# Optimization experiments

Measured on AMD Instinct MI355X. Metric: run time of the kernel, lower is better.

Reference implementation:

```python
import jax, jax.numpy as jnp
import numpy as np

N, CS, CZ = 512, 384, 128
H, C, PQ, PV = 12, 16, 4, 8
NB = 8
EPS = 1e-8


def _ln(x, g, b):
    m = jnp.mean(x, axis=-1, keepdims=True)
    v = jnp.mean((x - m) ** 2, axis=-1, keepdims=True)
    return (x - m) / jnp.sqrt(v + 1e-5) * g + b


def _quat_rot(bcd):
    # (1, b, c, d) quaternion -> rotation matrix, as in AF2 BackboneUpdate
    ones = jnp.ones(bcd.shape[:-1] + (1,), bcd.dtype)
    q = jnp.concatenate([ones, bcd], axis=-1)
    q = q / jnp.linalg.norm(q, axis=-1, keepdims=True)
    w, x, y, z = q[..., 0], q[..., 1], q[..., 2], q[..., 3]
    R = jnp.stack([
        1 - 2 * (y * y + z * z), 2 * (x * y - w * z), 2 * (x * z + w * y),
        2 * (x * y + w * z), 1 - 2 * (x * x + z * z), 2 * (y * z - w * x),
        2 * (x * z - w * y), 2 * (y * z + w * x), 1 - 2 * (x * x + y * y),
    ], axis=-1)
    return R.reshape(bcd.shape[:-1] + (3, 3))


def _ipa(s, z, R, t, p):
    n = s.shape[0]
    q = (s @ p['w_q']).reshape(n, H, C)
    kv = (s @ p['w_kv']).reshape(n, H, 2, C)
    k, v = kv[..., 0, :], kv[..., 1, :]

    # local points -> global frames
    q_pts = (s @ p['w_qpts']).reshape(n, H * PQ, 3)
    q_pts = jnp.einsum('nxy,npy->npx', R, q_pts) + t[:, None, :]
    q_pts = q_pts.reshape(n, H, PQ, 3)
    kv_pts = (s @ p['w_kvpts']).reshape(n, H * (PQ + PV), 3)
    kv_pts = jnp.einsum('nxy,npy->npx', R, kv_pts) + t[:, None, :]
    kv_pts = kv_pts.reshape(n, H, PQ + PV, 3)
    k_pts, v_pts = kv_pts[:, :, :PQ], kv_pts[:, :, PQ:]

    b = z @ p['w_b']  # [i, j, H]

    scalar = jnp.einsum('ihc,jhc->hij', q, k) / np.sqrt(C)
    # sum_p ||q_ip - k_jp||^2 expanded to avoid [N,N,H,P,3] intermediate
    sq_q = jnp.sum(q_pts ** 2, axis=(-1, -2)).T  # [H, i]
    sq_k = jnp.sum(k_pts ** 2, axis=(-1, -2)).T  # [H, j]
    cross = jnp.einsum('ihpc,jhpc->hij', q_pts, k_pts)
    d2 = sq_q[:, :, None] + sq_k[:, None, :] - 2.0 * cross  # [H, i, j]

    gamma = jax.nn.softplus(p['head_weights'])  # [H]
    w_C = np.sqrt(2.0 / (9.0 * PQ))
    w_L = np.sqrt(1.0 / 3.0)
    logits = w_L * (scalar + jnp.transpose(b, (2, 0, 1))
                    - gamma[:, None, None] * (w_C / 2.0) * d2)
    a = jax.nn.softmax(logits, axis=-1)  # [H, i, j]

    o = jnp.einsum('hij,jhc->ihc', a, v).reshape(n, H * C)
    o_pt = jnp.einsum('hij,jhpc->ihpc', a, v_pts)
    # back to local frame: R_i^{-1} (o_pt - t_i)
    o_pt = jnp.einsum('nyx,nhpy->nhpx', R, o_pt - t[:, None, None, :])
    o_pt_norm = jnp.sqrt(jnp.sum(o_pt ** 2, axis=-1) + EPS)  # [n, H, PV]
    o_pair = jnp.einsum('hij,ijz->ihz', a, z).reshape(n, H * CZ)

    cat = jnp.concatenate([o, o_pt.reshape(n, H * PV * 3),
                           o_pt_norm.reshape(n, H * PV), o_pair], axis=-1)
    return cat @ p['w_out'] + p['b_out']


def _forward(s, z, p):
    n = s.shape[0]
    R = jnp.broadcast_to(jnp.eye(3, dtype=s.dtype), (n, 3, 3))
    t = jnp.zeros((n, 3), s.dtype)
    for _ in range(NB):  # shared weights across blocks, as in AF2
        s = s + _ipa(s, z, R, t, p)
        s = _ln(s, p['ln1_g'], p['ln1_b'])
        h = jax.nn.relu(s @ p['w_t1'])
        h = jax.nn.relu(h @ p['w_t2'])
        s = s + h @ p['w_t3']
        s = _ln(s, p['ln2_g'], p['ln2_b'])
        upd = s @ p['w_bb'] + p['b_bb']  # [n, 6]
        Ru = _quat_rot(upd[:, :3])
        tu = upd[:, 3:]
        t = jnp.einsum('nxy,ny->nx', R, tu) + t
        R = jnp.einsum('nxy,nyz->nxz', R, Ru)
    return jnp.concatenate([s, t], axis=-1)  # [n, CS + 3]


def setup_inputs() -> dict:
    key = jax.random.key(0)
    ks = jax.random.split(key, 12)
    sc = 0.02
    cat_dim = H * C + H * PV * 3 + H * PV + H * CZ  # 2112
    return {
        's': jax.random.normal(ks[0], (N, CS), jnp.float32),
        'z': jax.random.normal(ks[1], (N, N, CZ), jnp.float32),
        'w_q': jax.random.normal(ks[2], (CS, H * C), jnp.float32) * sc,
        'w_kv': jax.random.normal(ks[3], (CS, H * 2 * C), jnp.float32) * sc,
        'w_qpts': jax.random.normal(ks[4], (CS, H * PQ * 3), jnp.float32) * sc,
        'w_kvpts': jax.random.normal(ks[5], (CS, H * (PQ + PV) * 3), jnp.float32) * sc,
        'w_b': jax.random.normal(ks[6], (CZ, H), jnp.float32) * sc,
        'head_weights': jnp.zeros((H,), jnp.float32),
        'w_out': jax.random.normal(ks[7], (cat_dim, CS), jnp.float32) * sc,
        'b_out': jnp.zeros((CS,), jnp.float32),
        'ln1_g': jnp.ones((CS,), jnp.float32),
        'ln1_b': jnp.zeros((CS,), jnp.float32),
        'w_t1': jax.random.normal(ks[8], (CS, CS), jnp.float32) * sc,
        'w_t2': jax.random.normal(ks[9], (CS, CS), jnp.float32) * sc,
        'w_t3': jax.random.normal(ks[10], (CS, CS), jnp.float32) * sc,
        'ln2_g': jnp.ones((CS,), jnp.float32),
        'ln2_b': jnp.zeros((CS,), jnp.float32),
        'w_bb': jax.random.normal(ks[11], (CS, 6), jnp.float32) * sc,
        'b_bb': jnp.zeros((6,), jnp.float32),
    }


def reference(s, z, w_q, w_kv, w_qpts, w_kvpts, w_b, head_weights, w_out,
              b_out, ln1_g, ln1_b, w_t1, w_t2, w_t3, ln2_g, ln2_b, w_bb, b_bb):
    p = dict(w_q=w_q, w_kv=w_kv, w_qpts=w_qpts, w_kvpts=w_kvpts, w_b=w_b,
             head_weights=head_weights, w_out=w_out, b_out=b_out,
             ln1_g=ln1_g, ln1_b=ln1_b, w_t1=w_t1, w_t2=w_t2, w_t3=w_t3,
             ln2_g=ln2_g, ln2_b=ln2_b, w_bb=w_bb, b_bb=b_bb)
    return _forward(s, z, p)
```

## Files before the change

### kernel.cpp

```cpp
#include <hip/hip_runtime.h>
#include <hip/hip_bf16.h>

constexpr int Nres = 512;
constexpr int Cs   = 384;
constexpr int Cz   = 128;
constexpr int NH   = 12;
constexpr int HC   = 16;
constexpr int NPQ  = 4;
constexpr int NPV  = 8;
constexpr int NBLK = 8;
constexpr int PROJD = NH*HC + NH*2*HC + NH*NPQ*3 + NH*(NPQ+NPV)*3;
constexpr int CATD = NH*HC + NH*NPV*3 + NH*NPV + NH*Cz;
constexpr float W_L  = 0.57735026918962576f;
constexpr float W_C2 = 0.11785113019775793f;

using u16 = unsigned short;
typedef __bf16 bf16x8 __attribute__((ext_vector_type(8)));
typedef float  f32x4  __attribute__((ext_vector_type(4)));

static inline int gdiv(int n, int b) { return (n + b - 1) / b; }

static __device__ __forceinline__ u16 f2bf(float x) {
    __hip_bfloat16 h = __float2bfloat16(x);
    return *reinterpret_cast<u16*>(&h);
}
static __device__ __forceinline__ float bf2f(u16 x) {
    return __bfloat162float(*reinterpret_cast<__hip_bfloat16*>(&x));
}

__global__ void k_init(const float* __restrict__ s_in, float* __restrict__ s_cur,
                       u16* __restrict__ s_bf,
                       float* __restrict__ R, float* __restrict__ t) {
    int idx = blockIdx.x * blockDim.x + threadIdx.x;
    if (idx < Nres * Cs) { float v = s_in[idx]; s_cur[idx] = v; s_bf[idx] = f2bf(v); }
    if (idx < Nres * 9) {
        int e = idx % 9;
        R[idx] = (e == 0 || e == 4 || e == 8) ? 1.f : 0.f;
    }
    if (idx < Nres * 3) t[idx] = 0.f;
}

__global__ void k_concatW(const float* __restrict__ w_q, const float* __restrict__ w_kv,
                          const float* __restrict__ w_qpts, const float* __restrict__ w_kvpts,
                          float* __restrict__ Wcat) {
    int idx = blockIdx.x * blockDim.x + threadIdx.x;
    if (idx >= Cs * PROJD) return;
    int k = idx / PROJD, n = idx - k * PROJD;
    float v;
    if      (n < 192) v = w_q[k * 192 + n];
    else if (n < 576) v = w_kv[k * 384 + (n - 192)];
    else if (n < 720) v = w_qpts[k * 144 + (n - 576)];
    else              v = w_kvpts[k * 432 + (n - 720)];
    Wcat[idx] = v;
}

__global__ void k_transposeW(const float* __restrict__ in, u16* __restrict__ out,
                             int K, int N) {
    __shared__ float tile[32][33];
    int n0 = blockIdx.x * 32, k0 = blockIdx.y * 32;
    int tx = threadIdx.x & 31, ty = threadIdx.x >> 5;
#pragma unroll
    for (int j = 0; j < 4; j++)
        tile[ty + j * 8][tx] = in[(size_t)(k0 + ty + j * 8) * N + n0 + tx];
    __syncthreads();
#pragma unroll
    for (int j = 0; j < 4; j++)
        out[(size_t)(n0 + ty + j * 8) * K + k0 + tx] = f2bf(tile[tx][ty + j * 8]);
}

__global__ void k_zT(const float* __restrict__ z, u16* __restrict__ zT) {
    __shared__ float tile[32][33];
    int i  = blockIdx.x;
    int j0 = blockIdx.y * 32;
    int c0 = blockIdx.z * 32;
    int tx = threadIdx.x & 31, ty = threadIdx.x >> 5;
    const float* src = z + (size_t)i * Nres * Cz;
#pragma unroll
    for (int l = 0; l < 4; l++)
        tile[ty + l * 8][tx] = src[(size_t)(j0 + ty + l * 8) * Cz + c0 + tx];
    __syncthreads();
    u16* dst = zT + (size_t)i * Cz * Nres;
#pragma unroll
    for (int l = 0; l < 4; l++)
        dst[(size_t)(c0 + ty + l * 8) * Nres + j0 + tx] = f2bf(tile[tx][ty + l * 8]);
}

__global__ void __launch_bounds__(256)
k_gemm_mfma(const u16* __restrict__ A, const u16* __restrict__ Bt,
            float* __restrict__ P, int M, int K, int N, int Kc) {
    __shared__ u16 As[64 * 40];
    __shared__ u16 Bs[64 * 40];
    const int tid = threadIdx.x;
    const int m0 = blockIdx.y * 64;
    const int n0 = blockIdx.x * 64;
    const int kbeg = blockIdx.z * Kc;
    const int wv = tid >> 6, lane = tid & 63;
    const int wm = (wv >> 1) * 32, wn = (wv & 1) * 32;
    const int lrow = lane & 15, lq = lane >> 4;

    f32x4 zero = {0.f, 0.f, 0.f, 0.f};
    f32x4 acc00 = zero, acc01 = zero, acc10 = zero, acc11 = zero;

    const int srow = tid >> 2;
    const int sko  = (tid & 3) * 8;

    for (int k0 = kbeg; k0 < kbeg + Kc; k0 += 32) {
        *(uint4*)&As[srow * 40 + sko] = *(const uint4*)&A[(size_t)(m0 + srow) * K + k0 + sko];
        *(uint4*)&Bs[srow * 40 + sko] = *(const uint4*)&Bt[(size_t)(n0 + srow) * K + k0 + sko];
        __syncthreads();
        bf16x8 a0 = *reinterpret_cast<const bf16x8*>(&As[(wm + lrow) * 40 + lq * 8]);
        bf16x8 a1 = *reinterpret_cast<const bf16x8*>(&As[(wm + 16 + lrow) * 40 + lq * 8]);
        bf16x8 b0 = *reinterpret_cast<const bf16x8*>(&Bs[(wn + lrow) * 40 + lq * 8]);
        bf16x8 b1 = *reinterpret_cast<const bf16x8*>(&Bs[(wn + 16 + lrow) * 40 + lq * 8]);
        acc00 = __builtin_amdgcn_mfma_f32_16x16x32_bf16(a0, b0, acc00, 0, 0, 0);
        acc01 = __builtin_amdgcn_mfma_f32_16x16x32_bf16(a0, b1, acc01, 0, 0, 0);
        acc10 = __builtin_amdgcn_mfma_f32_16x16x32_bf16(a1, b0, acc10, 0, 0, 0);
        acc11 = __builtin_amdgcn_mfma_f32_16x16x32_bf16(a1, b1, acc11, 0, 0, 0);
        __syncthreads();
    }
    float* Pp = P + (size_t)blockIdx.z * M * N;
    const int rbase = m0 + wm + lq * 4;
    const int cbase = n0 + wn + lrow;
#pragma unroll
    for (int r = 0; r < 4; r++) {
        Pp[(size_t)(rbase + r) * N + cbase]           = acc00[r];
        Pp[(size_t)(rbase + r) * N + cbase + 16]      = acc01[r];
        Pp[(size_t)(rbase + 16 + r) * N + cbase]      = acc10[r];
        Pp[(size_t)(rbase + 16 + r) * N + cbase + 16] = acc11[r];
    }
}

__global__ void __launch_bounds__(256)
k_gemm_rbf(const u16* __restrict__ A, const u16* __restrict__ Bt,
           float* __restrict__ outf, u16* __restrict__ outb,
           int M, int K, int N, int relu_bf) {
    __shared__ u16 As[32 * 40];
    __shared__ u16 Bs[64 * 40];
    const int tid = threadIdx.x;
    const int m0 = blockIdx.y * 32;
    const int n0 = blockIdx.x * 64;
    const int wv = tid >> 6, lane = tid & 63;
    const int wm = (wv >> 1) * 16, wn = (wv & 1) * 32;
    const int lrow = lane & 15, lq = lane >> 4;
    f32x4 zero = {0.f, 0.f, 0.f, 0.f};
    f32x4 acc0 = zero, acc1 = zero;
    const int srow = tid >> 2, sko = (tid & 3) * 8;
    for (int k0 = 0; k0 < K; k0 += 32) {
        if (tid < 128)
            *(uint4*)&As[srow * 40 + sko] = *(const uint4*)&A[(size_t)(m0 + srow) * K + k0 + sko];
        *(uint4*)&Bs[srow * 40 + sko] = *(const uint4*)&Bt[(size_t)(n0 + srow) * K + k0 + sko];
        __syncthreads();
        bf16x8 a  = *reinterpret_cast<const bf16x8*>(&As[(wm + lrow) * 40 + lq * 8]);
        bf16x8 b0 = *reinterpret_cast<const bf16x8*>(&Bs[(wn + lrow) * 40 + lq * 8]);
        bf16x8 b1 = *reinterpret_cast<const bf16x8*>(&Bs[(wn + 16 + lrow) * 40 + lq * 8]);
        acc0 = __builtin_amdgcn_mfma_f32_16x16x32_bf16(a, b0, acc0, 0, 0, 0);
        acc1 = __builtin_amdgcn_mfma_f32_16x16x32_bf16(a, b1, acc1, 0, 0, 0);
        __syncthreads();
    }
    const int rbase = m0 + wm + lq * 4;
    const int cbase = n0 + wn + lrow;
    if (relu_bf) {
#pragma unroll
        for (int r = 0; r < 4; r++) {
            outb[(size_t)(rbase + r) * N + cbase]      = f2bf(fmaxf(acc0[r], 0.f));
            outb[(size_t)(rbase + r) * N + cbase + 16] = f2bf(fmaxf(acc1[r], 0.f));
        }
    } else {
#pragma unroll
        for (int r = 0; r < 4; r++) {
            outf[(size_t)(rbase + r) * N + cbase]      = acc0[r];
            outf[(size_t)(rbase + r) * N + cbase + 16] = acc1[r];
        }
    }
}

__global__ void k_bproj(const float* __restrict__ z, const float* __restrict__ w_b,
                        float* __restrict__ b_hij) {
    __shared__ float zs[16][129];
    __shared__ float wbs[Cz * NH];
    const int tid = threadIdx.x;
    const int base = blockIdx.x * 16;
#pragma unroll
    for (int l = 0; l < 6; l++) {
        int idx = tid + l * 256;
        if (idx < Cz * NH) wbs[idx] = w_b[idx];
    }
#pragma unroll
    for (int l = 0; l < 8; l++) {
        int idx = tid + l * 256;
        int r = idx >> 7, c = idx & 127;
        zs[r][c] = z[(size_t)(base + r) * Cz + c];
    }
    __syncthreads();
    if (tid < 192) {
        int h = tid >> 4, r = tid & 15;
        float acc = 0.f;
        for (int c = 0; c < Cz; c++) acc += zs[r][c] * wbs[c * NH + h];
        int row = base + r;
        int i = row >> 9, j = row & 511;
        b_hij[((size_t)h * Nres + i) * Nres + j] = acc * W_L;
    }
}

__global__ void k_prep(const float* __restrict__ proj, const float* __restrict__ R,
                       const float* __restrict__ t, const float* __restrict__ hw,
                       u16* __restrict__ Aaug, u16* __restrict__ Baug,
                       u16* __restrict__ vhT) {
    int idx = blockIdx.x * blockDim.x + threadIdx.x;
    if (idx >= NH * Nres) return;
    int h = idx / Nres, i = idx % Nres;
    float R_[9], t_[3];
#pragma unroll
    for (int e = 0; e < 9; e++) R_[e] = R[i * 9 + e];
#pragma unroll
    for (int e = 0; e < 3; e++) t_[e] = t[i * 3 + e];
    const float* prow = proj + (size_t)i * PROJD;
    float gam = log1pf(__expf(hw[h]));
    float ch  = sqrtf(2.f * gam * W_C2);

    u16 arow[32], brow[32];
#pragma unroll
    for (int c = 0; c < HC; c++) {
        arow[c] = f2bf(prow[h * HC + c] * (W_L * 0.25f));
        brow[c] = f2bf(prow[192 + h * 2 * HC + c]);
        vhT[((size_t)h * 48 + c) * Nres + i] = f2bf(prow[192 + h * 2 * HC + HC + c]);
    }
#pragma unroll
    for (int p = 0; p < NPQ; p++) {
        const float* src = prow + 576 + (h * NPQ + p) * 3;
        float y0 = src[0], y1 = src[1], y2 = src[2];
        float v0 = R_[0]*y0 + R_[1]*y1 + R_[2]*y2 + t_[0];
        float v1 = R_[3]*y0 + R_[4]*y1 + R_[5]*y2 + t_[1];
        float v2 = R_[6]*y0 + R_[7]*y1 + R_[8]*y2 + t_[2];
        float s = W_L * ch;
        arow[16 + p*3 + 0] = f2bf(v0 * s);
        arow[16 + p*3 + 1] = f2bf(v1 * s);
        arow[16 + p*3 + 2] = f2bf(v2 * s);
    }
    float sk = 0.f;
#pragma unroll
    for (int p = 0; p < NPQ + NPV; p++) {
        const float* src = prow + 720 + (h * (NPQ+NPV) + p) * 3;
        float y0 = src[0], y1 = src[1], y2 = src[2];
        float v0 = R_[0]*y0 + R_[1]*y1 + R_[2]*y2 + t_[0];
        float v1 = R_[3]*y0 + R_[4]*y1 + R_[5]*y2 + t_[1];
        float v2 = R_[6]*y0 + R_[7]*y1 + R_[8]*y2 + t_[2];
        if (p < NPQ) {
            brow[16 + p*3 + 0] = f2bf(v0 * ch);
            brow[16 + p*3 + 1] = f2bf(v1 * ch);
            brow[16 + p*3 + 2] = f2bf(v2 * ch);
            sk += v0*v0 + v1*v1 + v2*v2;
        } else {
            int c0 = 16 + (p - NPQ) * 3;
            vhT[((size_t)h * 48 + c0 + 0) * Nres + i] = f2bf(v0);
            vhT[((size_t)h * 48 + c0 + 1) * Nres + i] = f2bf(v1);
            vhT[((size_t)h * 48 + c0 + 2) * Nres + i] = f2bf(v2);
        }
    }
    float x = -W_L * gam * W_C2 * sk;
    u16 hi = f2bf(x);
    float lo = x - bf2f(hi);
    arow[28] = f2bf(1.0f); arow[29] = f2bf(1.0f); arow[30] = 0; arow[31] = 0;
    brow[28] = hi;         brow[29] = f2bf(lo);   brow[30] = 0; brow[31] = 0;

    uint4* ad = (uint4*)&Aaug[((size_t)h * Nres + i) * 32];
    uint4* bd = (uint4*)&Baug[((size_t)h * Nres + i) * 32];
    const uint4* as = (const uint4*)arow;
    const uint4* bs = (const uint4*)brow;
#pragma unroll
    for (int e = 0; e < 4; e++) { ad[e] = as[e]; bd[e] = bs[e]; }
}

__global__ void __launch_bounds__(256)
k_qk(const u16* __restrict__ Aaug, const u16* __restrict__ Baug,
     const float* __restrict__ b_hij, float* __restrict__ S) {
    __shared__ u16 As[64 * 40];
    __shared__ u16 Bs[64 * 40];
    const int tid = threadIdx.x;
    const int h  = blockIdx.z;
    const int i0 = blockIdx.y * 64;
    const int j0 = blockIdx.x * 64;
    const int wv = tid >> 6, lane = tid & 63;
    const int wm = (wv >> 1) * 32, wn = (wv & 1) * 32;
    const int lrow = lane & 15, lq = lane >> 4;
    const int srow = tid >> 2, sko = (tid & 3) * 8;

    *(uint4*)&As[srow * 40 + sko] = *(const uint4*)&Aaug[((size_t)h * Nres + i0 + srow) * 32 + sko];
    *(uint4*)&Bs[srow * 40 + sko] = *(const uint4*)&Baug[((size_t)h * Nres + j0 + srow) * 32 + sko];
    __syncthreads();

    f32x4 zero = {0.f, 0.f, 0.f, 0.f};
    bf16x8 a0 = *reinterpret_cast<const bf16x8*>(&As[(wm + lrow) * 40 + lq * 8]);
    bf16x8 a1 = *reinterpret_cast<const bf16x8*>(&As[(wm + 16 + lrow) * 40 + lq * 8]);
    bf16x8 b0 = *reinterpret_cast<const bf16x8*>(&Bs[(wn + lrow) * 40 + lq * 8]);
    bf16x8 b1 = *reinterpret_cast<const bf16x8*>(&Bs[(wn + 16 + lrow) * 40 + lq * 8]);
    f32x4 acc00 = __builtin_amdgcn_mfma_f32_16x16x32_bf16(a0, b0, zero, 0, 0, 0);
    f32x4 acc01 = __builtin_amdgcn_mfma_f32_16x16x32_bf16(a0, b1, zero, 0, 0, 0);
    f32x4 acc10 = __builtin_amdgcn_mfma_f32_16x16x32_bf16(a1, b0, zero, 0, 0, 0);
    f32x4 acc11 = __builtin_amdgcn_mfma_f32_16x16x32_bf16(a1, b1, zero, 0, 0, 0);

    const float* bh = b_hij + ((size_t)h * Nres + i0) * Nres + j0;
    float* Sp = S + ((size_t)h * Nres + i0) * Nres + j0;
    const int rbase = wm + lq * 4;
    const int cbase = wn + lrow;
#pragma unroll
    for (int r = 0; r < 4; r++) {
        Sp[(size_t)(rbase + r) * Nres + cbase]           = acc00[r] + bh[(size_t)(rbase + r) * Nres + cbase];
        Sp[(size_t)(rbase + r) * Nres + cbase + 16]      = acc01[r] + bh[(size_t)(rbase + r) * Nres + cbase + 16];
        Sp[(size_t)(rbase + 16 + r) * Nres + cbase]      = acc10[r] + bh[(size_t)(rbase + 16 + r) * Nres + cbase];
        Sp[(size_t)(rbase + 16 + r) * Nres + cbase + 16] = acc11[r] + bh[(size_t)(rbase + 16 + r) * Nres + cbase + 16];
    }
}

__global__ void __launch_bounds__(256)
k_sm_opair(const float* __restrict__ S, const u16* __restrict__ zT,
           u16* __restrict__ Pbf, u16* __restrict__ cat_bf) {
    __shared__ u16 P_lds[16 * 520];
    __shared__ u16 Bs[128 * 40];
    const int i = blockIdx.x;
    const int tid = threadIdx.x;
    const int wv = tid >> 6, ln = tid & 63;

    for (int l = tid; l < 4 * 520; l += 256) P_lds[12 * 520 + l] = 0;

#pragma unroll
    for (int hh = 0; hh < 3; hh++) {
        int h = wv + hh * 4;
        const float* Srow = S + ((size_t)h * Nres + i) * Nres;
        float vals[8];
        float m = -1e30f;
#pragma unroll
        for (int jj = 0; jj < 8; jj++) { vals[jj] = Srow[ln + jj * 64]; m = fmaxf(m, vals[jj]); }
#pragma unroll
        for (int off = 32; off > 0; off >>= 1) m = fmaxf(m, __shfl_xor(m, off));
        float sm = 0.f;
#pragma unroll
        for (int jj = 0; jj < 8; jj++) { vals[jj] = __expf(vals[jj] - m); sm += vals[jj]; }
#pragma unroll
        for (int off = 32; off > 0; off >>= 1) sm += __shfl_xor(sm, off);
        float inv = 1.f / sm;
        u16* aP = Pbf + ((size_t)h * Nres + i) * Nres;
#pragma unroll
        for (int jj = 0; jj < 8; jj++) {
            u16 pb = f2bf(vals[jj] * inv);
            aP[ln + jj * 64] = pb;
            P_lds[h * 520 + ln + jj * 64] = pb;
        }
    }
    __syncthreads();

    const int lrow = ln & 15, lq = ln >> 4;
    const int wn = wv * 32;
    f32x4 zero = {0.f, 0.f, 0.f, 0.f};
    f32x4 acc0 = zero, acc1 = zero;
    const u16* Bp = zT + (size_t)i * Cz * Nres;
    const int srow = tid >> 2, sko = (tid & 3) * 8;
    for (int k0 = 0; k0 < Nres; k0 += 32) {
        *(uint4*)&Bs[srow * 40 + sko]        = *(const uint4*)&Bp[(size_t)srow * Nres + k0 + sko];
        *(uint4*)&Bs[(64 + srow) * 40 + sko] = *(const uint4*)&Bp[(size_t)(64 + srow) * Nres + k0 + sko];
        __syncthreads();
        bf16x8 a  = *reinterpret_cast<const bf16x8*>(&P_lds[lrow * 520 + k0 + lq * 8]);
        bf16x8 b0 = *reinterpret_cast<const bf16x8*>(&Bs[(wn + lrow) * 40 + lq * 8]);
        bf16x8 b1 = *reinterpret_cast<const bf16x8*>(&Bs[(wn + 16 + lrow) * 40 + lq * 8]);
        acc0 = __builtin_amdgcn_mfma_f32_16x16x32_bf16(a, b0, acc0, 0, 0, 0);
        acc1 = __builtin_amdgcn_mfma_f32_16x16x32_bf16(a, b1, acc1, 0, 0, 0);
        __syncthreads();
    }
    u16* crow = cat_bf + (size_t)i * CATD + 576;
#pragma unroll
    for (int r = 0; r < 4; r++) {
        int row = lq * 4 + r;
        if (row < NH) {
            crow[row * Cz + wn + lrow]      = f2bf(acc0[r]);
            crow[row * Cz + wn + 16 + lrow] = f2bf(acc1[r]);
        }
    }
}

__global__ void __launch_bounds__(256)
k_ov(const u16* __restrict__ Pbf, const u16* __restrict__ vhT,
     const float* __restrict__ R, const float* __restrict__ t,
     u16* __restrict__ cat_bf) {
    __shared__ u16 As[64 * 40];
    __shared__ u16 Bs[48 * 40];
    __shared__ float Ct[64 * 49];
    const int h  = blockIdx.x;
    const int i0 = blockIdx.y * 64;
    const int tid = threadIdx.x;
    const int wv = tid >> 6, lane = tid & 63;
    const int lrow = lane & 15, lq = lane >> 4;
    const int wm = wv * 16;
    f32x4 zero = {0.f, 0.f, 0.f, 0.f};
    f32x4 acc0 = zero, acc1 = zero, acc2 = zero;
    const u16* Ap = Pbf + (size_t)h * Nres * Nres + (size_t)i0 * Nres;
    const u16* Bp = vhT + (size_t)h * 48 * Nres;
    const int srow = tid >> 2, sko = (tid & 3) * 8;
    for (int k0 = 0; k0 < Nres; k0 += 32) {
        *(uint4*)&As[srow * 40 + sko] = *(const uint4*)&Ap[(size_t)srow * Nres + k0 + sko];
        if (tid < 192)
            *(uint4*)&Bs[srow * 40 + sko] = *(const uint4*)&Bp[(size_t)srow * Nres + k0 + sko];
        __syncthreads();
        bf16x8 a  = *reinterpret_cast<const bf16x8*>(&As[(wm + lrow) * 40 + lq * 8]);
        bf16x8 b0 = *reinterpret_cast<const bf16x8*>(&Bs[(lrow) * 40 + lq * 8]);
        bf16x8 b1 = *reinterpret_cast<const bf16x8*>(&Bs[(16 + lrow) * 40 + lq * 8]);
        bf16x8 b2 = *reinterpret_cast<const bf16x8*>(&Bs[(32 + lrow) * 40 + lq * 8]);
        acc0 = __builtin_amdgcn_mfma_f32_16x16x32_bf16(a, b0, acc0, 0, 0, 0);
        acc1 = __builtin_amdgcn_mfma_f32_16x16x32_bf16(a, b1, acc1, 0, 0, 0);
        acc2 = __builtin_amdgcn_mfma_f32_16x16x32_bf16(a, b2, acc2, 0, 0, 0);
        __syncthreads();
    }
#pragma unroll
    for (int r = 0; r < 4; r++) {
        int row = wm + lq * 4 + r;
        Ct[row * 49 + lrow]      = acc0[r];
        Ct[row * 49 + 16 + lrow] = acc1[r];
        Ct[row * 49 + 32 + lrow] = acc2[r];
    }
    __syncthreads();
#pragma unroll
    for (int l = 0; l < 4; l++) {
        int idx = tid + l * 256;
        int r = idx >> 4, c = idx & 15;
        cat_bf[(size_t)(i0 + r) * CATD + h * HC + c] = f2bf(Ct[r * 49 + c]);
    }
#pragma unroll
    for (int l = 0; l < 2; l++) {
        int idx = tid + l * 256;
        int r = idx >> 3, p = idx & 7;
        int i = i0 + r;
        float g0 = Ct[r * 49 + 16 + p * 3 + 0];
        float g1 = Ct[r * 49 + 16 + p * 3 + 1];
        float g2 = Ct[r * 49 + 16 + p * 3 + 2];
        float d0 = g0 - t[i * 3 + 0], d1 = g1 - t[i * 3 + 1], d2v = g2 - t[i * 3 + 2];
        const float* Rn = R + i * 9;
        float l0 = Rn[0] * d0 + Rn[3] * d1 + Rn[6] * d2v;
        float l1 = Rn[1] * d0 + Rn[4] * d1 + Rn[7] * d2v;
        float l2 = Rn[2] * d0 + Rn[5] * d1 + Rn[8] * d2v;
        int hp = h * NPV + p;
        u16* crow = cat_bf + (size_t)i * CATD;
        crow[192 + hp * 3 + 0] = f2bf(l0);
        crow[192 + hp * 3 + 1] = f2bf(l1);
        crow[192 + hp * 3 + 2] = f2bf(l2);
        crow[480 + hp] = f2bf(sqrtf(l0 * l0 + l1 * l1 + l2 * l2 + 1e-8f));
    }
}

__global__ void k_reduce_ln(const float* __restrict__ P, const float* __restrict__ bias,
                            float* __restrict__ s, u16* __restrict__ s_bf,
                            const float* __restrict__ g, const float* __restrict__ b,
                            int nsplit) {
    __shared__ float red[512];
    int i = blockIdx.x, tid = threadIdx.x;
    float v = s[(size_t)i * Cs + tid];
    if (bias) v += bias[tid];
    for (int sp = 0; sp < nsplit; sp++) v += P[(size_t)sp * Nres * Cs + (size_t)i * Cs + tid];
    red[tid] = v;
    if (tid < 128) red[384 + tid] = 0.f;
    __syncthreads();
    for (int st = 256; st > 0; st >>= 1) { if (tid < st) red[tid] += red[tid + st]; __syncthreads(); }
    float mean = red[0] / Cs;
    __syncthreads();
    float d = v - mean;
    red[tid] = d * d;
    if (tid < 128) red[384 + tid] = 0.f;
    __syncthreads();
    for (int st = 256; st > 0; st >>= 1) { if (tid < st) red[tid] += red[tid + st]; __syncthreads(); }
    float var = red[0] / Cs;
    float o = d * rsqrtf(var + 1e-5f) * g[tid] + b[tid];
    s[(size_t)i * Cs + tid] = o;
    s_bf[(size_t)i * Cs + tid] = f2bf(o);
}

__global__ void k_reduce_ln_bb(const float* __restrict__ P, float* __restrict__ s,
                               u16* __restrict__ s_bf,
                               const float* __restrict__ g, const float* __restrict__ b,
                               int nsplit,
                               const float* __restrict__ w_bb, const float* __restrict__ b_bb,
                               float* __restrict__ R, float* __restrict__ t) {
    __shared__ float red[512];
    __shared__ float uw[36];
    int i = blockIdx.x, tid = threadIdx.x;
    float v = s[(size_t)i * Cs + tid];
    for (int sp = 0; sp < nsplit; sp++) v += P[(size_t)sp * Nres * Cs + (size_t)i * Cs + tid];
    red[tid] = v;
    if (tid < 128) red[384 + tid] = 0.f;
    __syncthreads();
    for (int st = 256; st > 0; st >>= 1) { if (tid < st) red[tid] += red[tid + st]; __syncthreads(); }
    float mean = red[0] / Cs;
    __syncthreads();
    float d = v - mean;
    red[tid] = d * d;
    if (tid < 128) red[384 + tid] = 0.f;
    __syncthreads();
    for (int st = 256; st > 0; st >>= 1) { if (tid < st) red[tid] += red[tid + st]; __syncthreads(); }
    float var = red[0] / Cs;
    float o = d * rsqrtf(var + 1e-5f) * g[tid] + b[tid];
    s[(size_t)i * Cs + tid] = o;
    s_bf[(size_t)i * Cs + tid] = f2bf(o);

    float u[6];
#pragma unroll
    for (int dd = 0; dd < 6; dd++) u[dd] = o * w_bb[tid * 6 + dd];
#pragma unroll
    for (int off = 32; off > 0; off >>= 1)
#pragma unroll
        for (int dd = 0; dd < 6; dd++) u[dd] += __shfl_xor(u[dd], off);
    int wv = tid >> 6, lane = tid & 63;
    if (lane == 0) {
#pragma unroll
        for (int dd = 0; dd < 6; dd++) uw[wv * 6 + dd] = u[dd];
    }
    __syncthreads();
    if (tid == 0) {
        float uu[6];
#pragma unroll
        for (int dd = 0; dd < 6; dd++) {
            float a = b_bb[dd];
            for (int w = 0; w < 6; w++) a += uw[w * 6 + dd];
            uu[dd] = a;
        }
        float qb = uu[0], qc = uu[1], qd = uu[2];
        float inv = rsqrtf(1.f + qb*qb + qc*qc + qd*qd);
        float w = inv, x = qb * inv, y = qc * inv, zq = qd * inv;
        float Ru[9] = {
            1.f - 2.f*(y*y + zq*zq), 2.f*(x*y - w*zq),       2.f*(x*zq + w*y),
            2.f*(x*y + w*zq),        1.f - 2.f*(x*x + zq*zq), 2.f*(y*zq - w*x),
            2.f*(x*zq - w*y),        2.f*(y*zq + w*x),        1.f - 2.f*(x*x + y*y)
        };
        float Ro[9];
#pragma unroll
        for (int e = 0; e < 9; e++) Ro[e] = R[i * 9 + e];
        float tu0 = uu[3], tu1 = uu[4], tu2 = uu[5];
        t[i*3+0] += Ro[0]*tu0 + Ro[1]*tu1 + Ro[2]*tu2;
        t[i*3+1] += Ro[3]*tu0 + Ro[4]*tu1 + Ro[5]*tu2;
        t[i*3+2] += Ro[6]*tu0 + Ro[7]*tu1 + Ro[8]*tu2;
#pragma unroll
        for (int r = 0; r < 3; r++)
#pragma unroll
            for (int c = 0; c < 3; c++)
                R[i*9 + r*3 + c] = Ro[r*3+0]*Ru[0*3+c] + Ro[r*3+1]*Ru[1*3+c] + Ro[r*3+2]*Ru[2*3+c];
    }
}

__global__ void k_final(const float* __restrict__ s, const float* __restrict__ t,
                        float* __restrict__ out) {
    int idx = blockIdx.x * blockDim.x + threadIdx.x;
    if (idx >= Nres * (Cs + 3)) return;
    int i = idx / (Cs + 3), c = idx - i * (Cs + 3);
    out[idx] = (c < Cs) ? s[(size_t)i * Cs + c] : t[i * 3 + (c - Cs)];
}

extern "C" void kernel_launch(void* const* d_in, const int* in_sizes, int n_in,
                              void* d_out, int out_size, void* d_ws, size_t ws_size,
                              hipStream_t stream) {
    const float* s_in    = (const float*)d_in[0];
    const float* z       = (const float*)d_in[1];
    const float* w_q     = (const float*)d_in[2];
    const float* w_kv    = (const float*)d_in[3];
    const float* w_qpts  = (const float*)d_in[4];
    const float* w_kvpts = (const float*)d_in[5];
    const float* w_b     = (const float*)d_in[6];
    const float* hw      = (const float*)d_in[7];
    const float* w_out   = (const float*)d_in[8];
    const float* b_out   = (const float*)d_in[9];
    const float* ln1_g   = (const float*)d_in[10];
    const float* ln1_b   = (const float*)d_in[11];
    const float* w_t1    = (const float*)d_in[12];
    const float* w_t2    = (const float*)d_in[13];
    const float* w_t3    = (const float*)d_in[14];
    const float* ln2_g   = (const float*)d_in[15];
    const float* ln2_b   = (const float*)d_in[16];
    const float* w_bb    = (const float*)d_in[17];
    const float* b_bb    = (const float*)d_in[18];
    float* out = (float*)d_out;

    float* ws = (float*)d_ws;
    size_t off = 0;
    float* s_cur = ws + off; off += (size_t)Nres * Cs;
    float* b_hij = ws + off; off += (size_t)NH * Nres * Nres;
    float* proj  = ws + off; off += (size_t)Nres * PROJD;
    float* Wcat  = ws + off; off += (size_t)Cs * PROJD;
    float* Rbuf  = ws + off; off += (size_t)Nres * 9;
    float* tbuf  = ws + off; off += (size_t)Nres * 3;
    float* Pslab = ws + off; off += (size_t)11 * Nres * Cs;
    float* Sbuf  = ws + off; off += (size_t)NH * Nres * Nres;
    u16* s_bf   = (u16*)(ws + off); off += (size_t)Nres * Cs / 2;
    u16* cat_bf = (u16*)(ws + off); off += (size_t)Nres * CATD / 2;
    u16* h1_bf  = (u16*)(ws + off); off += (size_t)Nres * Cs / 2;
    u16* h2_bf  = (u16*)(ws + off); off += (size_t)Nres * Cs / 2;
    u16* WcatT  = (u16*)(ws + off); off += (size_t)Cs * PROJD / 2;
    u16* w_outT = (u16*)(ws + off); off += (size_t)CATD * Cs / 2;
    u16* w_t1T  = (u16*)(ws + off); off += (size_t)Cs * Cs / 2;
    u16* w_t2T  = (u16*)(ws + off); off += (size_t)Cs * Cs / 2;
    u16* w_t3T  = (u16*)(ws + off); off += (size_t)Cs * Cs / 2;
    u16* Pbf    = (u16*)(ws + off); off += (size_t)NH * Nres * Nres / 2;
    u16* vhTbf  = (u16*)(ws + off); off += (size_t)NH * 48 * Nres / 2;
    u16* Aaug   = (u16*)(ws + off); off += (size_t)NH * Nres * 32 / 2;
    u16* Baug   = (u16*)(ws + off); off += (size_t)NH * Nres * 32 / 2;
    u16* zTbf   = (u16*)(ws + off); off += (size_t)Nres * Cz * Nres / 2;

    k_init<<<gdiv(Nres*Cs, 256), 256, 0, stream>>>(s_in, s_cur, s_bf, Rbuf, tbuf);
    k_concatW<<<gdiv(Cs*PROJD, 256), 256, 0, stream>>>(w_q, w_kv, w_qpts, w_kvpts, Wcat);
    k_transposeW<<<dim3(PROJD/32, Cs/32), 256, 0, stream>>>(Wcat, WcatT, Cs, PROJD);
    k_transposeW<<<dim3(Cs/32, CATD/32), 256, 0, stream>>>(w_out, w_outT, CATD, Cs);
    k_transposeW<<<dim3(Cs/32, Cs/32), 256, 0, stream>>>(w_t1, w_t1T, Cs, Cs);
    k_transposeW<<<dim3(Cs/32, Cs/32), 256, 0, stream>>>(w_t2, w_t2T, Cs, Cs);
    k_transposeW<<<dim3(Cs/32, Cs/32), 256, 0, stream>>>(w_t3, w_t3T, Cs, Cs);
    k_bproj<<<Nres*Nres/16, 256, 0, stream>>>(z, w_b, b_hij);
    k_zT<<<dim3(Nres, Nres/32, Cz/32), 256, 0, stream>>>(z, zTbf);

    for (int it = 0; it < NBLK; it++) {
        k_gemm_rbf<<<dim3(PROJD/64, Nres/32), 256, 0, stream>>>(s_bf, WcatT, proj, nullptr, Nres, Cs, PROJD, 0);
        k_prep<<<gdiv(NH*Nres, 256), 256, 0, stream>>>(proj, Rbuf, tbuf, hw, Aaug, Baug, vhTbf);
        k_qk<<<dim3(Nres/64, Nres/64, NH), 256, 0, stream>>>(Aaug, Baug, b_hij, Sbuf);
        k_sm_opair<<<Nres, 256, 0, stream>>>(Sbuf, zTbf, Pbf, cat_bf);
        k_ov<<<dim3(NH, Nres/64), 256, 0, stream>>>(Pbf, vhTbf, Rbuf, tbuf, cat_bf);
        k_gemm_mfma<<<dim3(Cs/64, Nres/64, 11), 256, 0, stream>>>(cat_bf, w_outT, Pslab, Nres, CATD, Cs, 192);
        k_reduce_ln<<<Nres, Cs, 0, stream>>>(Pslab, b_out, s_cur, s_bf, ln1_g, ln1_b, 11);
        k_gemm_rbf<<<dim3(Cs/64, Nres/32), 256, 0, stream>>>(s_bf, w_t1T, nullptr, h1_bf, Nres, Cs, Cs, 1);
        k_gemm_rbf<<<dim3(Cs/64, Nres/32), 256, 0, stream>>>(h1_bf, w_t2T, nullptr, h2_bf, Nres, Cs, Cs, 1);
        k_gemm_rbf<<<dim3(Cs/64, Nres/32), 256, 0, stream>>>(h2_bf, w_t3T, Pslab, nullptr, Nres, Cs, Cs, 0);
        k_reduce_ln_bb<<<Nres, Cs, 0, stream>>>(Pslab, s_cur, s_bf, ln2_g, ln2_b, 1, w_bb, b_bb, Rbuf, tbuf);
    }

    k_final<<<gdiv(Nres*(Cs+3), 256), 256, 0, stream>>>(s_cur, tbuf, out);
}
```

Before: 1.025 ms.

## Double-buffer LDS tiles in MFMA GEMM loops and reduce split-K factor

New measurement: 948.3 us. 1.08x faster.

```diff
diff --git a/kernel.cpp b/kernel.cpp
--- a/kernel.cpp
+++ b/kernel.cpp
@@ -88,12 +88,13 @@
 __global__ void __launch_bounds__(256)
 k_gemm_mfma(const u16* __restrict__ A, const u16* __restrict__ Bt,
             float* __restrict__ P, int M, int K, int N, int Kc) {
-    __shared__ u16 As[64 * 40];
-    __shared__ u16 Bs[64 * 40];
+    __shared__ u16 As[2][64 * 40];
+    __shared__ u16 Bs[2][64 * 40];
     const int tid = threadIdx.x;
     const int m0 = blockIdx.y * 64;
     const int n0 = blockIdx.x * 64;
     const int kbeg = blockIdx.z * Kc;
+    const int kend = kbeg + Kc;
     const int wv = tid >> 6, lane = tid & 63;
     const int wm = (wv >> 1) * 32, wn = (wv & 1) * 32;
     const int lrow = lane & 15, lq = lane >> 4;
@@ -103,20 +104,36 @@
 
     const int srow = tid >> 2;
     const int sko  = (tid & 3) * 8;
-
-    for (int k0 = kbeg; k0 < kbeg + Kc; k0 += 32) {
-        *(uint4*)&As[srow * 40 + sko] = *(const uint4*)&A[(size_t)(m0 + srow) * K + k0 + sko];
-        *(uint4*)&Bs[srow * 40 + sko] = *(const uint4*)&Bt[(size_t)(n0 + srow) * K + k0 + sko];
-        __syncthreads();
-        bf16x8 a0 = *reinterpret_cast<const bf16x8*>(&As[(wm + lrow) * 40 + lq * 8]);
-        bf16x8 a1 = *reinterpret_cast<const bf16x8*>(&As[(wm + 16 + lrow) * 40 + lq * 8]);
-        bf16x8 b0 = *reinterpret_cast<const bf16x8*>(&Bs[(wn + lrow) * 40 + lq * 8]);
-        bf16x8 b1 = *reinterpret_cast<const bf16x8*>(&Bs[(wn + 16 + lrow) * 40 + lq * 8]);
+    const size_t aoff = (size_t)(m0 + srow) * K + sko;
+    const size_t boff = (size_t)(n0 + srow) * K + sko;
+
+    uint4 ra = *(const uint4*)&A[aoff + kbeg];
+    uint4 rb = *(const uint4*)&Bt[boff + kbeg];
+    *(uint4*)&As[0][srow * 40 + sko] = ra;
+    *(uint4*)&Bs[0][srow * 40 + sko] = rb;
+    __syncthreads();
+
+    int buf = 0;
+    for (int k0 = kbeg; k0 < kend; k0 += 32) {
+        const bool nxt = (k0 + 32 < kend);
+        if (nxt) {
+            ra = *(const uint4*)&A[aoff + k0 + 32];
+            rb = *(const uint4*)&Bt[boff + k0 + 32];
+        }
+        bf16x8 a0 = *reinterpret_cast<const bf16x8*>(&As[buf][(wm + lrow) * 40 + lq * 8]);
+        bf16x8 a1 = *reinterpret_cast<const bf16x8*>(&As[buf][(wm + 16 + lrow) * 40 + lq * 8]);
+        bf16x8 b0 = *reinterpret_cast<const bf16x8*>(&Bs[buf][(wn + lrow) * 40 + lq * 8]);
+        bf16x8 b1 = *reinterpret_cast<const bf16x8*>(&Bs[buf][(wn + 16 + lrow) * 40 + lq * 8]);
         acc00 = __builtin_amdgcn_mfma_f32_16x16x32_bf16(a0, b0, acc00, 0, 0, 0);
         acc01 = __builtin_amdgcn_mfma_f32_16x16x32_bf16(a0, b1, acc01, 0, 0, 0);
         acc10 = __builtin_amdgcn_mfma_f32_16x16x32_bf16(a1, b0, acc10, 0, 0, 0);
         acc11 = __builtin_amdgcn_mfma_f32_16x16x32_bf16(a1, b1, acc11, 0, 0, 0);
-        __syncthreads();
+        if (nxt) {
+            *(uint4*)&As[buf ^ 1][srow * 40 + sko] = ra;
+            *(uint4*)&Bs[buf ^ 1][srow * 40 + sko] = rb;
+            __syncthreads();
+            buf ^= 1;
+        }
     }
     float* Pp = P + (size_t)blockIdx.z * M * N;
     const int rbase = m0 + wm + lq * 4;
@@ -134,8 +151,8 @@
 k_gemm_rbf(const u16* __restrict__ A, const u16* __restrict__ Bt,
            float* __restrict__ outf, u16* __restrict__ outb,
            int M, int K, int N, int relu_bf) {
-    __shared__ u16 As[32 * 40];
-    __shared__ u16 Bs[64 * 40];
+    __shared__ u16 As[2][32 * 40];
+    __shared__ u16 Bs[2][64 * 40];
     const int tid = threadIdx.x;
     const int m0 = blockIdx.y * 32;
     const int n0 = blockIdx.x * 64;
@@ -145,17 +162,34 @@
     f32x4 zero = {0.f, 0.f, 0.f, 0.f};
     f32x4 acc0 = zero, acc1 = zero;
     const int srow = tid >> 2, sko = (tid & 3) * 8;
+    const size_t aoff = (size_t)(m0 + srow) * K + sko;
+    const size_t boff = (size_t)(n0 + srow) * K + sko;
+
+    uint4 ra, rb;
+    if (tid < 128) ra = *(const uint4*)&A[aoff];
+    rb = *(const uint4*)&Bt[boff];
+    if (tid < 128) *(uint4*)&As[0][srow * 40 + sko] = ra;
+    *(uint4*)&Bs[0][srow * 40 + sko] = rb;
+    __syncthreads();
+
+    int buf = 0;
     for (int k0 = 0; k0 < K; k0 += 32) {
-        if (tid < 128)
-            *(uint4*)&As[srow * 40 + sko] = *(const uint4*)&A[(size_t)(m0 + srow) * K + k0 + sko];
-        *(uint4*)&Bs[srow * 40 + sko] = *(const uint4*)&Bt[(size_t)(n0 + srow) * K + k0 + sko];
-        __syncthreads();
-        bf16x8 a  = *reinterpret_cast<const bf16x8*>(&As[(wm + lrow) * 40 + lq * 8]);
-        bf16x8 b0 = *reinterpret_cast<const bf16x8*>(&Bs[(wn + lrow) * 40 + lq * 8]);
-        bf16x8 b1 = *reinterpret_cast<const bf16x8*>(&Bs[(wn + 16 + lrow) * 40 + lq * 8]);
+        const bool nxt = (k0 + 32 < K);
+        if (nxt) {
+            if (tid < 128) ra = *(const uint4*)&A[aoff + k0 + 32];
+            rb = *(const uint4*)&Bt[boff + k0 + 32];
+        }
+        bf16x8 a  = *reinterpret_cast<const bf16x8*>(&As[buf][(wm + lrow) * 40 + lq * 8]);
+        bf16x8 b0 = *reinterpret_cast<const bf16x8*>(&Bs[buf][(wn + lrow) * 40 + lq * 8]);
+        bf16x8 b1 = *reinterpret_cast<const bf16x8*>(&Bs[buf][(wn + 16 + lrow) * 40 + lq * 8]);
         acc0 = __builtin_amdgcn_mfma_f32_16x16x32_bf16(a, b0, acc0, 0, 0, 0);
         acc1 = __builtin_amdgcn_mfma_f32_16x16x32_bf16(a, b1, acc1, 0, 0, 0);
-        __syncthreads();
+        if (nxt) {
+            if (tid < 128) *(uint4*)&As[buf ^ 1][srow * 40 + sko] = ra;
+            *(uint4*)&Bs[buf ^ 1][srow * 40 + sko] = rb;
+            __syncthreads();
+            buf ^= 1;
+        }
     }
     const int rbase = m0 + wm + lq * 4;
     const int cbase = n0 + wn + lrow;
@@ -316,10 +350,17 @@
 k_sm_opair(const float* __restrict__ S, const u16* __restrict__ zT,
            u16* __restrict__ Pbf, u16* __restrict__ cat_bf) {
     __shared__ u16 P_lds[16 * 520];
-    __shared__ u16 Bs[128 * 40];
+    __shared__ u16 Bs[2][128 * 40];
     const int i = blockIdx.x;
     const int tid = threadIdx.x;
     const int wv = tid >> 6, ln = tid & 63;
+    const int srow = tid >> 2, sko = (tid & 3) * 8;
+    const u16* Bp = zT + (size_t)i * Cz * Nres;
+    const size_t b0off = (size_t)srow * Nres + sko;
+    const size_t b1off = (size_t)(64 + srow) * Nres + sko;
+
+    uint4 rb0 = *(const uint4*)&Bp[b0off];
+    uint4 rb1 = *(const uint4*)&Bp[b1off];
 
     for (int l = tid; l < 4 * 520; l += 256) P_lds[12 * 520 + l] = 0;
 
@@ -347,24 +388,32 @@
             P_lds[h * 520 + ln + jj * 64] = pb;
         }
     }
+    *(uint4*)&Bs[0][srow * 40 + sko]        = rb0;
+    *(uint4*)&Bs[0][(64 + srow) * 40 + sko] = rb1;
     __syncthreads();
 
     const int lrow = ln & 15, lq = ln >> 4;
     const int wn = wv * 32;
     f32x4 zero = {0.f, 0.f, 0.f, 0.f};
     f32x4 acc0 = zero, acc1 = zero;
-    const u16* Bp = zT + (size_t)i * Cz * Nres;
-    const int srow = tid >> 2, sko = (tid & 3) * 8;
+    int buf = 0;
     for (int k0 = 0; k0 < Nres; k0 += 32) {
-        *(uint4*)&Bs[srow * 40 + sko]        = *(const uint4*)&Bp[(size_t)srow * Nres + k0 + sko];
-        *(uint4*)&Bs[(64 + srow) * 40 + sko] = *(const uint4*)&Bp[(size_t)(64 + srow) * Nres + k0 + sko];
-        __syncthreads();
+        const bool nxt = (k0 + 32 < Nres);
+        if (nxt) {
+            rb0 = *(const uint4*)&Bp[b0off + k0 + 32];
+            rb1 = *(const uint4*)&Bp[b1off + k0 + 32];
+        }
         bf16x8 a  = *reinterpret_cast<const bf16x8*>(&P_lds[lrow * 520 + k0 + lq * 8]);
-        bf16x8 b0 = *reinterpret_cast<const bf16x8*>(&Bs[(wn + lrow) * 40 + lq * 8]);
-        bf16x8 b1 = *reinterpret_cast<const bf16x8*>(&Bs[(wn + 16 + lrow) * 40 + lq * 8]);
+        bf16x8 b0 = *reinterpret_cast<const bf16x8*>(&Bs[buf][(wn + lrow) * 40 + lq * 8]);
+        bf16x8 b1 = *reinterpret_cast<const bf16x8*>(&Bs[buf][(wn + 16 + lrow) * 40 + lq * 8]);
         acc0 = __builtin_amdgcn_mfma_f32_16x16x32_bf16(a, b0, acc0, 0, 0, 0);
         acc1 = __builtin_amdgcn_mfma_f32_16x16x32_bf16(a, b1, acc1, 0, 0, 0);
-        __syncthreads();
+        if (nxt) {
+            *(uint4*)&Bs[buf ^ 1][srow * 40 + sko]        = rb0;
+            *(uint4*)&Bs[buf ^ 1][(64 + srow) * 40 + sko] = rb1;
+            __syncthreads();
+            buf ^= 1;
+        }
     }
     u16* crow = cat_bf + (size_t)i * CATD + 576;
 #pragma unroll
@@ -381,8 +430,8 @@
 k_ov(const u16* __restrict__ Pbf, const u16* __restrict__ vhT,
      const float* __restrict__ R, const float* __restrict__ t,
      u16* __restrict__ cat_bf) {
-    __shared__ u16 As[64 * 40];
-    __shared__ u16 Bs[48 * 40];
+    __shared__ u16 As[2][64 * 40];
+    __shared__ u16 Bs[2][48 * 40];
     __shared__ float Ct[64 * 49];
     const int h  = blockIdx.x;
     const int i0 = blockIdx.y * 64;
@@ -395,19 +444,36 @@
     const u16* Ap = Pbf + (size_t)h * Nres * Nres + (size_t)i0 * Nres;
     const u16* Bp = vhT + (size_t)h * 48 * Nres;
     const int srow = tid >> 2, sko = (tid & 3) * 8;
+    const size_t aoff = (size_t)srow * Nres + sko;
+    const size_t boff = (size_t)srow * Nres + sko;
+
+    uint4 ra, rb;
+    ra = *(const uint4*)&Ap[aoff];
+    if (tid < 192) rb = *(const uint4*)&Bp[boff];
+    *(uint4*)&As[0][srow * 40 + sko] = ra;
+    if (tid < 192) *(uint4*)&Bs[0][srow * 40 + sko] = rb;
+    __syncthreads();
+
+    int buf = 0;
     for (int k0 = 0; k0 < Nres; k0 += 32) {
-        *(uint4*)&As[srow * 40 + sko] = *(const uint4*)&Ap[(size_t)srow * Nres + k0 + sko];
-        if (tid < 192)
-            *(uint4*)&Bs[srow * 40 + sko] = *(const uint4*)&Bp[(size_t)srow * Nres + k0 + sko];
-        __syncthreads();
-        bf16x8 a  = *reinterpret_cast<const bf16x8*>(&As[(wm + lrow) * 40 + lq * 8]);
-        bf16x8 b0 = *reinterpret_cast<const bf16x8*>(&Bs[(lrow) * 40 + lq * 8]);
-        bf16x8 b1 = *reinterpret_cast<const bf16x8*>(&Bs[(16 + lrow) * 40 + lq * 8]);
-        bf16x8 b2 = *reinterpret_cast<const bf16x8*>(&Bs[(32 + lrow) * 40 + lq * 8]);
+        const bool nxt = (k0 + 32 < Nres);
+        if (nxt) {
+            ra = *(const uint4*)&Ap[aoff + k0 + 32];
+            if (tid < 192) rb = *(const uint4*)&Bp[boff + k0 + 32];
+        }
+        bf16x8 a  = *reinterpret_cast<const bf16x8*>(&As[buf][(wm + lrow) * 40 + lq * 8]);
+        bf16x8 b0 = *reinterpret_cast<const bf16x8*>(&Bs[buf][(lrow) * 40 + lq * 8]);
+        bf16x8 b1 = *reinterpret_cast<const bf16x8*>(&Bs[buf][(16 + lrow) * 40 + lq * 8]);
+        bf16x8 b2 = *reinterpret_cast<const bf16x8*>(&Bs[buf][(32 + lrow) * 40 + lq * 8]);
         acc0 = __builtin_amdgcn_mfma_f32_16x16x32_bf16(a, b0, acc0, 0, 0, 0);
         acc1 = __builtin_amdgcn_mfma_f32_16x16x32_bf16(a, b1, acc1, 0, 0, 0);
         acc2 = __builtin_amdgcn_mfma_f32_16x16x32_bf16(a, b2, acc2, 0, 0, 0);
-        __syncthreads();
+        if (nxt) {
+            *(uint4*)&As[buf ^ 1][srow * 40 + sko] = ra;
+            if (tid < 192) *(uint4*)&Bs[buf ^ 1][srow * 40 + sko] = rb;
+            __syncthreads();
+            buf ^= 1;
+        }
     }
 #pragma unroll
     for (int r = 0; r < 4; r++) {
@@ -615,8 +681,8 @@
         k_qk<<<dim3(Nres/64, Nres/64, NH), 256, 0, stream>>>(Aaug, Baug, b_hij, Sbuf);
         k_sm_opair<<<Nres, 256, 0, stream>>>(Sbuf, zTbf, Pbf, cat_bf);
         k_ov<<<dim3(NH, Nres/64), 256, 0, stream>>>(Pbf, vhTbf, Rbuf, tbuf, cat_bf);
-        k_gemm_mfma<<<dim3(Cs/64, Nres/64, 11), 256, 0, stream>>>(cat_bf, w_outT, Pslab, Nres, CATD, Cs, 192);
-        k_reduce_ln<<<Nres, Cs, 0, stream>>>(Pslab, b_out, s_cur, s_bf, ln1_g, ln1_b, 11);
+        k_gemm_mfma<<<dim3(Cs/64, Nres/64, 6), 256, 0, stream>>>(cat_bf, w_outT, Pslab, Nres, CATD, Cs, 352);
+        k_reduce_ln<<<Nres, Cs, 0, stream>>>(Pslab, b_out, s_cur, s_bf, ln1_g, ln1_b, 6);
         k_gemm_rbf<<<dim3(Cs/64, Nres/32), 256, 0, stream>>>(s_bf, w_t1T, nullptr, h1_bf, Nres, Cs, Cs, 1);
         k_gemm_rbf<<<dim3(Cs/64, Nres/32), 256, 0, stream>>>(h1_bf, w_t2T, nullptr, h2_bf, Nres, Cs, Cs, 1);
         k_gemm_rbf<<<dim3(Cs/64, Nres/32), 256, 0, stream>>>(h2_bf, w_t3T, Pslab, nullptr, Nres, Cs, Cs, 0);
```
